# Performance work log

Hardware: AMD Instinct MI355X
Metric: run time of the kernel (lower is better)

## Reference

```python
import jax, jax.numpy as jnp
import numpy as np

B, CIN, CF, FH, FW = 16, 512, 64, 11, 20
N = 2784          # anchors
NOFF = 72         # S offsets
D = CF * FH       # 704

def setup_inputs() -> dict:
    key = jax.random.key(0)
    ks = jax.random.split(key, 12)
    x = jax.random.normal(ks[0], (B, CIN, FH, FW), jnp.float32)
    conv_w = jax.random.normal(ks[1], (CF, CIN), jnp.float32) * 0.02
    conv_b = jax.random.normal(ks[2], (CF,), jnp.float32) * 0.01
    attn_w = jax.random.normal(ks[3], (N - 1, D), jnp.float32) * 0.02
    attn_b = jnp.zeros((N - 1,), jnp.float32)
    cls_w = jax.random.normal(ks[4], (2, 2 * D), jnp.float32) * 0.02
    cls_b = jnp.zeros((2,), jnp.float32)
    reg_w = jax.random.normal(ks[5], (NOFF + 1, 2 * D), jnp.float32) * 0.02
    reg_b = jnp.zeros((NOFF + 1,), jnp.float32)
    anchors = jax.random.normal(ks[6], (N, 5 + NOFF), jnp.float32)
    # emulate compute_anchor_cut_indices: per-anchor per-fmap-row x index, some invalid
    unclamped = jax.random.randint(ks[7], (N, FH), -3, FW + 3, jnp.int32)
    invalid_mask = (unclamped < 0) | (unclamped > FW)
    cut_xs = jnp.clip(unclamped, 0, FW - 1).astype(jnp.int32)
    return {"x": x, "conv_w": conv_w, "conv_b": conv_b, "attn_w": attn_w,
            "attn_b": attn_b, "cls_w": cls_w, "cls_b": cls_b, "reg_w": reg_w,
            "reg_b": reg_b, "anchors": anchors, "cut_xs": cut_xs,
            "invalid_mask": invalid_mask}

def reference(x, conv_w, conv_b, attn_w, attn_b, cls_w, cls_b, reg_w, reg_b,
              anchors, cut_xs, invalid_mask):
    # 1x1 conv: [B, CF, FH, FW]
    feat = jnp.einsum('bchw,oc->bohw', x, conv_w) + conv_b[None, :, None, None]
    # cut_anchor_features: gather per-anchor column of features, mask invalid
    ys = jnp.arange(FH)[None, :]                      # [1, FH] broadcasts with cut_xs [N, FH]
    rois = feat[:, :, ys, cut_xs]                     # [B, CF, N, FH]
    rois = jnp.where(invalid_mask[None, None], 0.0, rois)
    anchor_feat = jnp.transpose(rois, (0, 2, 1, 3)).reshape(B, N, D)  # (C-major, then H)
    # attention scores over other anchors
    scores = anchor_feat.reshape(B * N, D) @ attn_w.T + attn_b
    att = jax.nn.softmax(scores, axis=1).reshape(B, N, N - 1)
    # build NxN matrix: zero diagonal, off-diagonal filled row-wise with att
    r = jnp.arange(N)[:, None]
    c = jnp.arange(N)[None, :]
    k = jnp.clip(c - (c > r).astype(jnp.int32), 0, N - 2)  # [N, N]
    M = att[:, r, k] * (c != r)                       # [B, N, N]
    att_feat = jnp.einsum('bij,bjd->bid', M, anchor_feat)
    comb = jnp.concatenate([att_feat, anchor_feat], axis=-1)  # [B, N, 2D]
    cls = comb @ cls_w.T + cls_b                      # [B, N, 2]
    reg = comb @ reg_w.T + reg_b                      # [B, N, 73]
    mid = jnp.broadcast_to(anchors[None, :, 2:4], (B, N, 2))
    props = jnp.concatenate([cls, mid, anchors[None, :, 4:] + reg], axis=-1)  # [B, N, 77]
    return props, M
```

## Files before the change

kernel.cpp:

```cpp
#include <hip/hip_runtime.h>

#define B_    16
#define CIN_  512
#define CF_   64
#define FH_   11
#define FW_   20
#define N_    2784
#define NM1_  2783
#define D_    704
#define D2_   1408
#define ROWS_ 44544
#define PW_   77

#define NX_     1802240
#define NCW_    32768
#define NCB_    64
#define NATTW_  1959232
#define NATTB_  2783
#define NCLSW_  2816
#define NCLSB_  2
#define NREGW_  102784
#define NREGB_  73
#define NANCH_  214368
#define NCUT_   30624

#define OFF_FLAGS   0u
#define OFF_FEAT    256u
#define OFF_CANON   (1u<<20)
#define C_X      0u
#define C_ATTW   3604480u
#define C_CW     7522944u
#define C_ANCH   7588480u
#define C_CLSW   8017216u
#define C_REGW   8022848u
#define C_CB     8228416u
#define C_ATTB   8228544u
#define C_CLSB   8234112u
#define C_REGB   8234128u
#define C_CUT    8234288u
#define C_MASK   8356784u

typedef __bf16 bf16x8 __attribute__((ext_vector_type(8)));
typedef float  f32x4  __attribute__((ext_vector_type(4)));

typedef __attribute__((address_space(1))) void g_void;
typedef __attribute__((address_space(3))) void l_void;
#define GLD16(gp, lp) __builtin_amdgcn_global_load_lds((g_void*)(gp), (l_void*)(lp), 16, 0, 0)

__device__ __forceinline__ float bf2f(unsigned short u) {
    union { unsigned int u; float f; } v; v.u = ((unsigned int)u) << 16; return v.f;
}
__device__ __forceinline__ unsigned short f2bf(float f) {
    union { float f; unsigned int u; } v; v.f = f;
    unsigned int x = v.u;
    return (unsigned short)((x + 0x7FFFu + ((x >> 16) & 1u)) >> 16);
}

__device__ __forceinline__ int swz8(int olid, int nwg) {
    int xcd = olid & 7, pos = olid >> 3;
    int q = nwg >> 3, r = nwg & 7;
    int off = (xcd < r) ? xcd * (q + 1) : r * (q + 1) + (xcd - r) * q;
    return off + pos;
}

__global__ __launch_bounds__(256) void k_detect(const unsigned int* __restrict__ attw,
                                                const unsigned int* __restrict__ cut,
                                                const unsigned int* __restrict__ msk,
                                                int* __restrict__ flags) {
    __shared__ int cnt[3];
    int t = threadIdx.x;
    if (t < 3) cnt[t] = 0;
    __syncthreads();
    int c0 = 0, c1 = 0, c2 = 0;
    for (int i = t; i < 2048; i += 256) {
        unsigned int e = (attw[i] >> 7) & 0xFFu;
        if (e >= 127u) c0++;
    }
    for (int i = t; i < 4096; i += 256) if (cut[i] >= 32u) c1++;
    for (int i = t; i < 4096; i += 256) if (msk[i] >= 2u)  c2++;
    atomicAdd(&cnt[0], c0); atomicAdd(&cnt[1], c1); atomicAdd(&cnt[2], c2);
    __syncthreads();
    if (t == 0) {
        flags[0] = cnt[0] > 64;
        flags[1] = cnt[1] > 64;
        flags[2] = cnt[2] > 64;
        flags[3] = 0;
    }
}

__device__ __forceinline__ void cvt_arr(const void* s, unsigned short* d, int n, int isf32,
                                        int tid, int stride) {
    if (isf32) {
        const float* p = (const float*)s;
        for (int i = tid; i < n; i += stride) d[i] = f2bf(p[i]);
    } else {
        const unsigned short* p = (const unsigned short*)s;
        for (int i = tid; i < n; i += stride) d[i] = p[i];
    }
}

__global__ __launch_bounds__(256) void k_canon_f(const void* sx, const void* scw, const void* scb,
                                                 const void* sattw, const void* sattb,
                                                 const void* sclsw, const void* sclsb,
                                                 const void* sregw, const void* sregb,
                                                 const void* sanch, char* canon,
                                                 const int* __restrict__ flags) {
    const int isf32 = flags[0];
    const int tid = blockIdx.x * 256 + threadIdx.x;
    const int stride = gridDim.x * 256;
    cvt_arr(sx,    (unsigned short*)(canon + C_X),    NX_,    isf32, tid, stride);
    cvt_arr(sattw, (unsigned short*)(canon + C_ATTW), NATTW_, isf32, tid, stride);
    cvt_arr(scw,   (unsigned short*)(canon + C_CW),   NCW_,   isf32, tid, stride);
    cvt_arr(sanch, (unsigned short*)(canon + C_ANCH), NANCH_, isf32, tid, stride);
    cvt_arr(sclsw, (unsigned short*)(canon + C_CLSW), NCLSW_, isf32, tid, stride);
    cvt_arr(sregw, (unsigned short*)(canon + C_REGW), NREGW_, isf32, tid, stride);
    cvt_arr(scb,   (unsigned short*)(canon + C_CB),   NCB_,   isf32, tid, stride);
    cvt_arr(sattb, (unsigned short*)(canon + C_ATTB), NATTB_, isf32, tid, stride);
    cvt_arr(sclsb, (unsigned short*)(canon + C_CLSB), NCLSB_, isf32, tid, stride);
    cvt_arr(sregb, (unsigned short*)(canon + C_REGB), NREGB_, isf32, tid, stride);
}

__global__ __launch_bounds__(256) void k_canon_i(const void* scut, const void* smsk,
                                                 char* canon, const int* __restrict__ flags) {
    const int cutb = flags[1], mskb = flags[2];
    int* ccut = (int*)(canon + C_CUT);
    int* cmsk = (int*)(canon + C_MASK);
    const int tid = blockIdx.x * 256 + threadIdx.x;
    const int stride = gridDim.x * 256;
    for (int i = tid; i < NCUT_; i += stride) {
        ccut[i] = cutb ? (int)((const unsigned char*)scut)[i] : ((const int*)scut)[i];
        int m = mskb ? (int)((const unsigned char*)smsk)[i] : ((const int*)smsk)[i];
        cmsk[i] = (m != 0);
    }
}

__global__ __launch_bounds__(256) void k_conv(const unsigned short* __restrict__ x,
                                              const unsigned short* __restrict__ cw,
                                              const unsigned short* __restrict__ cb,
                                              float* __restrict__ feat) {
    int idx = blockIdx.x * 256 + threadIdx.x;
    int w = idx % FW_;
    int h = (idx / FW_) % FH_;
    int o = (idx / (FW_ * FH_)) % CF_;
    int b = idx / (FW_ * FH_ * CF_);
    const unsigned short* xp = x + ((size_t)(b * CIN_) * FH_ + h) * FW_ + w;
    const unsigned short* wp = cw + (size_t)o * CIN_;
    float acc = bf2f(cb[o]);
#pragma unroll 8
    for (int c = 0; c < CIN_; ++c)
        acc += bf2f(xp[(size_t)c * (FH_ * FW_)]) * bf2f(wp[c]);
    feat[idx] = acc;
}

__global__ __launch_bounds__(256) void k_gather_af(const float* __restrict__ feat,
                                                   const int* __restrict__ cut,
                                                   const int* __restrict__ inv,
                                                   unsigned short* __restrict__ AF,
                                                   int batch_base) {
    int n = blockIdx.x, bl = blockIdx.y;
    int b = batch_base + bl;
    __shared__ int cu[FH_];
    __shared__ int iv[FH_];
    int t = threadIdx.x;
    if (t < FH_) { cu[t] = cut[n * FH_ + t]; iv[t] = inv[n * FH_ + t]; }
    __syncthreads();
    unsigned short* out = AF + ((size_t)(bl * N_ + n)) * D_;
    for (int d = t; d < D_; d += 256) {
        int c = d / FH_, h = d - c * FH_;
        float v = iv[h] ? 0.f : feat[((b * CF_ + c) * FH_ + h) * FW_ + cu[h]];
        out[d] = f2bf(v);
    }
}

__global__ __launch_bounds__(256) void k_gather_aft(const float* __restrict__ feat,
                                                    const int* __restrict__ cut,
                                                    const int* __restrict__ inv,
                                                    unsigned short* __restrict__ AFT,
                                                    int batch_base) {
    int d = blockIdx.x, bl = blockIdx.y;
    int b = batch_base + bl;
    int c = d / FH_, h = d - c * FH_;
    const float* fp = feat + ((b * CF_ + c) * FH_ + h) * FW_;
    unsigned short* out = AFT + ((size_t)(bl * D_ + d)) * N_;
    for (int n = threadIdx.x; n < N_; n += 256) {
        int w = cut[n * FH_ + h];
        float v = inv[n * FH_ + h] ? 0.f : fp[w];
        out[n] = f2bf(v);
    }
}

__global__ __launch_bounds__(256, 2) void k_scores(const unsigned short* __restrict__ AF,
                                                   const unsigned short* __restrict__ attw,
                                                   const unsigned short* __restrict__ attb,
                                                   unsigned short* __restrict__ Mbf,
                                                   int nloc) {
    __shared__ __bf16 As[2][256 * 32];
    __shared__ __bf16 Bs[2][128 * 32];
    const int t = threadIdx.x;
    const int nwg = gridDim.x * gridDim.y;
    const int olid = blockIdx.x + gridDim.x * blockIdx.y;
    const int nid = swz8(olid, nwg);
    const int jt = nid % 22, it = nid / 22;
    const int i0 = it * 256, j0 = jt * 128;
    const int lane = t & 63, wv = t >> 6;
    const int wrow = wv >> 1, wcol = wv & 1;
    const int l15 = lane & 15;
    const int hix = (((lane >> 4) ^ ((l15 >> 1) & 3)) * 8);

    f32x4 zero = {0.f, 0.f, 0.f, 0.f};
    f32x4 acc[8][4];
#pragma unroll
    for (int m = 0; m < 8; ++m)
#pragma unroll
        for (int n = 0; n < 4; ++n) acc[m][n] = zero;

    const unsigned short* aP[4];
    const unsigned short* bP[2];
#pragma unroll
    for (int k = 0; k < 4; ++k) {
        int s = t + 256 * k;
        int row = s >> 2;
        int ac = (((s & 3) ^ ((s >> 3) & 3)) * 8);
        int ir = i0 + row; if (ir > nloc - 1) ir = nloc - 1;
        aP[k] = AF + (size_t)ir * D_ + ac;
    }
#pragma unroll
    for (int k = 0; k < 2; ++k) {
        int s = t + 256 * k;
        int row = s >> 2;
        int ac = (((s & 3) ^ ((s >> 3) & 3)) * 8);
        int jr = j0 + row; if (jr > NM1_ - 1) jr = NM1_ - 1;
        bP[k] = attw + (size_t)jr * D_ + ac;
    }

    const int NT = D_ / 32;
#pragma unroll
    for (int k = 0; k < 4; ++k) GLD16(aP[k], As[0] + (t + 256 * k) * 8);
#pragma unroll
    for (int k = 0; k < 2; ++k) GLD16(bP[k], Bs[0] + (t + 256 * k) * 8);

    for (int kt = 0; kt < NT; ++kt) {
        const int cur = kt & 1;
        if (kt + 1 < NT) {
            const int nk = (kt + 1) * 32;
#pragma unroll
            for (int k = 0; k < 4; ++k) GLD16(aP[k] + nk, As[cur ^ 1] + (t + 256 * k) * 8);
#pragma unroll
            for (int k = 0; k < 2; ++k) GLD16(bP[k] + nk, Bs[cur ^ 1] + (t + 256 * k) * 8);
            asm volatile("s_waitcnt vmcnt(6)" ::: "memory");
        } else {
            asm volatile("s_waitcnt vmcnt(0)" ::: "memory");
        }
        __builtin_amdgcn_sched_barrier(0);
        __builtin_amdgcn_s_barrier();
        bf16x8 a[8], bb[4];
#pragma unroll
        for (int m = 0; m < 8; ++m)
            a[m] = *(const bf16x8*)(As[cur] + (wrow * 128 + m * 16 + l15) * 32 + hix);
#pragma unroll
        for (int n = 0; n < 4; ++n)
            bb[n] = *(const bf16x8*)(Bs[cur] + (wcol * 64 + n * 16 + l15) * 32 + hix);
#pragma unroll
        for (int m = 0; m < 8; ++m)
#pragma unroll
            for (int n = 0; n < 4; ++n)
                acc[m][n] = __builtin_amdgcn_mfma_f32_16x16x32_bf16(a[m], bb[n], acc[m][n], 0, 0, 0);
        __builtin_amdgcn_s_barrier();
        __builtin_amdgcn_sched_barrier(0);
    }

#pragma unroll
    for (int m = 0; m < 8; ++m) {
        int ib = i0 + wrow * 128 + m * 16 + (lane >> 4) * 4;
#pragma unroll
        for (int n = 0; n < 4; ++n) {
            int j = j0 + wcol * 64 + n * 16 + l15;
            if (j < NM1_) {
                float bias = bf2f(attb[j]);
#pragma unroll
                for (int q = 0; q < 4; ++q) {
                    int ii = ib + q;
                    if (ii < nloc) {
                        int r = ii % N_;
                        int c = j + (j >= r);
                        Mbf[(size_t)ii * N_ + c] = f2bf(acc[m][n][q] + bias);
                    }
                }
            }
        }
    }
}

__global__ __launch_bounds__(256) void k_softmax(unsigned short* __restrict__ Mbf,
                                                 float* __restrict__ Mout,
                                                 int row_base) {
    const int il = blockIdx.x;
    const int r = il % N_;
    unsigned short* srow = Mbf + (size_t)il * N_;
    float* orow = Mout + (size_t)(row_base + il) * N_;
    const int t = threadIdx.x;
    float f[16];
#pragma unroll
    for (int q = 0; q < 2; ++q) {
        int c8 = t + 256 * q;
        if (c8 < N_ / 8) {
            uint4 u = *(const uint4*)(srow + c8 * 8);
            const unsigned short* pu = (const unsigned short*)&u;
#pragma unroll
            for (int e = 0; e < 8; ++e) {
                int c = c8 * 8 + e;
                float v = bf2f(pu[e]);
                f[q * 8 + e] = (c == r) ? -1e30f : v;
            }
        } else {
#pragma unroll
            for (int e = 0; e < 8; ++e) f[q * 8 + e] = -1e30f;
        }
    }
    float m = -1e30f;
#pragma unroll
    for (int q = 0; q < 16; ++q) m = fmaxf(m, f[q]);
#pragma unroll
    for (int off = 32; off >= 1; off >>= 1) m = fmaxf(m, __shfl_xor(m, off, 64));
    __shared__ float red[4];
    if ((t & 63) == 0) red[t >> 6] = m;
    __syncthreads();
    m = fmaxf(fmaxf(red[0], red[1]), fmaxf(red[2], red[3]));

    float s = 0.f;
#pragma unroll
    for (int q = 0; q < 16; ++q) { float e = __expf(f[q] - m); f[q] = e; s += e; }
#pragma unroll
    for (int off = 32; off >= 1; off >>= 1) s += __shfl_xor(s, off, 64);
    __shared__ float red2[4];
    if ((t & 63) == 0) red2[t >> 6] = s;
    __syncthreads();
    s = red2[0] + red2[1] + red2[2] + red2[3];
    float inv = 1.0f / s;
#pragma unroll
    for (int q = 0; q < 2; ++q) {
        int c8 = t + 256 * q;
        if (c8 < N_ / 8) {
            float o[8];
            union { unsigned short u[8]; uint4 v; } pb;
#pragma unroll
            for (int e = 0; e < 8; ++e) {
                o[e] = f[q * 8 + e] * inv;
                pb.u[e] = f2bf(o[e]);
            }
            float4 o0 = {o[0], o[1], o[2], o[3]};
            float4 o1 = {o[4], o[5], o[6], o[7]};
            *(float4*)(orow + c8 * 8) = o0;
            *(float4*)(orow + c8 * 8 + 4) = o1;
            *(uint4*)(srow + c8 * 8) = pb.v;
        }
    }
}

__global__ __launch_bounds__(256, 2) void k_attgemm(const unsigned short* __restrict__ Mbf,
                                                    const unsigned short* __restrict__ AFT,
                                                    unsigned short* __restrict__ ATF) {
    __shared__ __bf16 As[2][256 * 32];
    __shared__ __bf16 Bs[2][128 * 32];
    const int t = threadIdx.x;
    const int nwg = gridDim.x * gridDim.y * gridDim.z;
    const int olid = blockIdx.x + gridDim.x * (blockIdx.y + gridDim.y * blockIdx.z);
    const int nid = swz8(olid, nwg);
    const int jt = nid % 6, it = (nid / 6) % 11, bl = nid / 66;
    const int i0 = it * 256, j0 = jt * 128;
    const int lane = t & 63, wv = t >> 6;
    const int wrow = wv >> 1, wcol = wv & 1;
    const int l15 = lane & 15;
    const int hix = (((lane >> 4) ^ ((l15 >> 1) & 3)) * 8);

    f32x4 zero = {0.f, 0.f, 0.f, 0.f};
    f32x4 acc[8][4];
#pragma unroll
    for (int m = 0; m < 8; ++m)
#pragma unroll
        for (int n = 0; n < 4; ++n) acc[m][n] = zero;

    const unsigned short* aP[4];
    const unsigned short* bP[2];
#pragma unroll
    for (int k = 0; k < 4; ++k) {
        int s = t + 256 * k;
        int row = s >> 2;
        int ac = (((s & 3) ^ ((s >> 3) & 3)) * 8);
        int ir = i0 + row; if (ir > N_ - 1) ir = N_ - 1;
        aP[k] = Mbf + ((size_t)bl * N_ + ir) * N_ + ac;
    }
#pragma unroll
    for (int k = 0; k < 2; ++k) {
        int s = t + 256 * k;
        int row = s >> 2;
        int ac = (((s & 3) ^ ((s >> 3) & 3)) * 8);
        int jr = j0 + row; if (jr > D_ - 1) jr = D_ - 1;
        bP[k] = AFT + (size_t)(bl * D_ + jr) * N_ + ac;
    }

    const int NT = N_ / 32;
#pragma unroll
    for (int k = 0; k < 4; ++k) GLD16(aP[k], As[0] + (t + 256 * k) * 8);
#pragma unroll
    for (int k = 0; k < 2; ++k) GLD16(bP[k], Bs[0] + (t + 256 * k) * 8);

    for (int kt = 0; kt < NT; ++kt) {
        const int cur = kt & 1;
        if (kt + 1 < NT) {
            const int nk = (kt + 1) * 32;
#pragma unroll
            for (int k = 0; k < 4; ++k) GLD16(aP[k] + nk, As[cur ^ 1] + (t + 256 * k) * 8);
#pragma unroll
            for (int k = 0; k < 2; ++k) GLD16(bP[k] + nk, Bs[cur ^ 1] + (t + 256 * k) * 8);
            asm volatile("s_waitcnt vmcnt(6)" ::: "memory");
        } else {
            asm volatile("s_waitcnt vmcnt(0)" ::: "memory");
        }
        __builtin_amdgcn_sched_barrier(0);
        __builtin_amdgcn_s_barrier();
        bf16x8 a[8], bb[4];
#pragma unroll
        for (int m = 0; m < 8; ++m)
            a[m] = *(const bf16x8*)(As[cur] + (wrow * 128 + m * 16 + l15) * 32 + hix);
#pragma unroll
        for (int n = 0; n < 4; ++n)
            bb[n] = *(const bf16x8*)(Bs[cur] + (wcol * 64 + n * 16 + l15) * 32 + hix);
#pragma unroll
        for (int m = 0; m < 8; ++m)
#pragma unroll
            for (int n = 0; n < 4; ++n)
                acc[m][n] = __builtin_amdgcn_mfma_f32_16x16x32_bf16(a[m], bb[n], acc[m][n], 0, 0, 0);
        __builtin_amdgcn_s_barrier();
        __builtin_amdgcn_sched_barrier(0);
    }

#pragma unroll
    for (int m = 0; m < 8; ++m) {
        int rb = i0 + wrow * 128 + m * 16 + (lane >> 4) * 4;
#pragma unroll
        for (int n = 0; n < 4; ++n) {
            int d = j0 + wcol * 64 + n * 16 + l15;
            if (d < D_) {
#pragma unroll
                for (int q = 0; q < 4; ++q) {
                    int rr = rb + q;
                    if (rr < N_)
                        ATF[((size_t)(bl * N_ + rr)) * D_ + d] = f2bf(acc[m][n][q]);
                }
            }
        }
    }
}

__global__ __launch_bounds__(256) void k_head(const unsigned short* __restrict__ ATF,
                                              const unsigned short* __restrict__ AF,
                                              const unsigned short* __restrict__ clsw,
                                              const unsigned short* __restrict__ clsb,
                                              const unsigned short* __restrict__ regw,
                                              const unsigned short* __restrict__ regb,
                                              const unsigned short* __restrict__ anch,
                                              float* __restrict__ props,
                                              int row_base, int nloc) {
    __shared__ __bf16 As[128 * 32];
    __shared__ __bf16 Ws[80 * 32];
    const int t = threadIdx.x;
    const int i0 = blockIdx.x * 128;
    const int lane = t & 63, wv = t >> 6;
    const int l15 = lane & 15, hi8 = (lane >> 4) * 8;

    f32x4 zero = {0.f, 0.f, 0.f, 0.f};
    f32x4 acc[2][5];
#pragma unroll
    for (int m = 0; m < 2; ++m)
#pragma unroll
        for (int n = 0; n < 5; ++n) acc[m][n] = zero;

    const int s0 = t, s1 = t + 256;
    const int ar0 = s0 >> 2, ac0 = (s0 & 3) * 8;
    const int ar1 = s1 >> 2, ac1 = (s1 & 3) * 8;
    int ir0 = i0 + ar0; if (ir0 > nloc - 1) ir0 = nloc - 1;
    int ir1 = i0 + ar1; if (ir1 > nloc - 1) ir1 = nloc - 1;
    const unsigned short* w0base = (ar0 < 2) ? (clsw + (size_t)ar0 * D2_)
                                             : (regw + (size_t)(ar0 - 2) * D2_);
    int r1 = 64 + (t >> 2);
    int rc = r1 < 75 ? r1 : 74;
    const unsigned short* w1base = regw + (size_t)(rc - 2) * D2_;
    const int w1c = (t & 3) * 8;

    for (int p = 0; p < 2; ++p) {
        const unsigned short* Asrc = (p == 0) ? ATF : AF;
        const int wcol = p * D_;
        for (int k0 = 0; k0 < D_; k0 += 32) {
            GLD16(Asrc + (size_t)ir0 * D_ + ac0 + k0, As + s0 * 8);
            GLD16(Asrc + (size_t)ir1 * D_ + ac1 + k0, As + s1 * 8);
            GLD16(w0base + wcol + k0 + ac0, Ws + s0 * 8);
            if (t < 64) GLD16(w1base + wcol + k0 + w1c, Ws + (size_t)(256 + t) * 8);
            __syncthreads();
            bf16x8 a[2], bb[5];
#pragma unroll
            for (int m = 0; m < 2; ++m)
                a[m] = *(const bf16x8*)(As + (wv * 32 + m * 16 + l15) * 32 + hi8);
#pragma unroll
            for (int n = 0; n < 5; ++n)
                bb[n] = *(const bf16x8*)(Ws + (n * 16 + l15) * 32 + hi8);
#pragma unroll
            for (int m = 0; m < 2; ++m)
#pragma unroll
                for (int n = 0; n < 5; ++n)
                    acc[m][n] = __builtin_amdgcn_mfma_f32_16x16x32_bf16(a[m], bb[n], acc[m][n], 0, 0, 0);
            __syncthreads();
        }
    }

#pragma unroll
    for (int m = 0; m < 2; ++m) {
        int ib = i0 + wv * 32 + m * 16 + (lane >> 4) * 4;
#pragma unroll
        for (int n = 0; n < 5; ++n) {
            int j = n * 16 + l15;
            if (j < 75) {
#pragma unroll
                for (int q = 0; q < 4; ++q) {
                    int i = ib + q;
                    if (i < nloc) {
                        size_t g = (size_t)(row_base + i);
                        int nn = i % N_;
                        float v = acc[m][n][q];
                        if (j < 2) {
                            props[g * PW_ + j] = v + bf2f(clsb[j]);
                            props[g * PW_ + 2 + j] = bf2f(anch[(size_t)nn * PW_ + 2 + j]);
                        } else {
                            int tt = j - 2;
                            props[g * PW_ + 4 + tt] = v + bf2f(regb[tt]) + bf2f(anch[(size_t)nn * PW_ + 4 + tt]);
                        }
                    }
                }
            }
        }
    }
}

extern "C" void kernel_launch(void* const* d_in, const int* in_sizes, int n_in,
                              void* d_out, int out_size, void* d_ws, size_t ws_size,
                              hipStream_t stream) {
    (void)in_sizes; (void)n_in; (void)out_size;

    float* props = (float*)d_out;
    float* Mbuf  = props + (size_t)ROWS_ * PW_;

    char* ws = (char*)d_ws;
    int* flags = (int*)(ws + OFF_FLAGS);
    float* feat = (float*)(ws + OFF_FEAT);
    char* canon = ws + OFF_CANON;
    unsigned short* cx    = (unsigned short*)(canon + C_X);
    unsigned short* cattw = (unsigned short*)(canon + C_ATTW);
    unsigned short* ccw   = (unsigned short*)(canon + C_CW);
    unsigned short* canch = (unsigned short*)(canon + C_ANCH);
    unsigned short* cclsw = (unsigned short*)(canon + C_CLSW);
    unsigned short* cregw = (unsigned short*)(canon + C_REGW);
    unsigned short* ccb   = (unsigned short*)(canon + C_CB);
    unsigned short* cattb = (unsigned short*)(canon + C_ATTB);
    unsigned short* cclsb = (unsigned short*)(canon + C_CLSB);
    unsigned short* cregb = (unsigned short*)(canon + C_REGB);
    int* ccut = (int*)(canon + C_CUT);
    int* cmsk = (int*)(canon + C_MASK);

    const size_t base = (size_t)(12u << 20);
    const size_t sAF  = (size_t)N_ * D_ * 2;
    const size_t sMB  = (size_t)N_ * N_ * 2;
    const size_t per  = 3 * sAF + sMB;
    int CN = 1;
    for (int c = 16; c >= 1; c >>= 1)
        if (ws_size >= base + (size_t)c * per) { CN = c; break; }
    unsigned short* AF  = (unsigned short*)(ws + base);
    unsigned short* AFT = AF  + (size_t)CN * N_ * D_;
    unsigned short* ATF = AFT + (size_t)CN * N_ * D_;
    unsigned short* Mbf = ATF + (size_t)CN * N_ * D_;

    k_detect<<<dim3(1), dim3(256), 0, stream>>>((const unsigned int*)d_in[3],
                                                (const unsigned int*)d_in[10],
                                                (const unsigned int*)d_in[11], flags);
    k_canon_f<<<dim3(1024), dim3(256), 0, stream>>>(d_in[0], d_in[1], d_in[2], d_in[3], d_in[4],
                                                    d_in[5], d_in[6], d_in[7], d_in[8], d_in[9],
                                                    canon, flags);
    k_canon_i<<<dim3(120), dim3(256), 0, stream>>>(d_in[10], d_in[11], canon, flags);
    k_conv<<<dim3(880), dim3(256), 0, stream>>>(cx, ccw, ccb, feat);

    const int nchunk = 16 / CN;
    for (int c = 0; c < nchunk; ++c) {
        const int bb = c * CN;
        const int rb = bb * N_;
        const int nl = CN * N_;
        const int it128 = (nl + 127) / 128;
        const int it256 = (nl + 255) / 256;
        const int atiles = (N_ + 255) / 256;
        k_gather_af<<<dim3(N_, CN), dim3(256), 0, stream>>>(feat, ccut, cmsk, AF, bb);
        k_gather_aft<<<dim3(D_, CN), dim3(256), 0, stream>>>(feat, ccut, cmsk, AFT, bb);
        k_scores<<<dim3(22, it256), dim3(256), 0, stream>>>(AF, cattw, cattb, Mbf, nl);
        k_softmax<<<dim3(nl), dim3(256), 0, stream>>>(Mbf, Mbuf, rb);
        k_attgemm<<<dim3(6, atiles, CN), dim3(256), 0, stream>>>(Mbf, AFT, ATF);
        k_head<<<dim3(it128), dim3(256), 0, stream>>>(ATF, AF, cclsw, cclsb, cregw, cregb,
                                                      canch, props, rb, nl);
    }
}
```

Before: 1.067 ms.

## Enlarge GEMM tiles to 256x256x64 with 512 threads and pad K to 2816

Both MFMA GEMMs (scores and attention-feature) move from 256x128 tiles with a K step of 32 and 256 threads to 256x256 tiles with a K step of 64, 512 threads and 8 waves. The LDS layout gets a new XOR swizzle for the wider rows. The Mbf and AFT buffers are padded to a row stride of 2816, with zero-filled tails written by softmax and gather, so the attention GEMM K loop divides evenly into 64-wide steps. The intent is more data reuse per loaded tile and fewer barriers per FLOP. In exchange it uses 128KB of LDS per block, runs one block per CU, and waits on vmcnt(0) at every step, which may reduce latency hiding.

New measurement: 1.097 ms. 1.03x slower.

```diff
diff --git a/kernel.cpp b/kernel.cpp
--- a/kernel.cpp
+++ b/kernel.cpp
@@ -7,6 +7,7 @@
 #define FW_   20
 #define N_    2784
 #define NM1_  2783
+#define PK_   2816
 #define D_    704
 #define D2_   1408
 #define ROWS_ 44544
@@ -181,31 +182,33 @@
     int b = batch_base + bl;
     int c = d / FH_, h = d - c * FH_;
     const float* fp = feat + ((b * CF_ + c) * FH_ + h) * FW_;
-    unsigned short* out = AFT + ((size_t)(bl * D_ + d)) * N_;
-    for (int n = threadIdx.x; n < N_; n += 256) {
-        int w = cut[n * FH_ + h];
-        float v = inv[n * FH_ + h] ? 0.f : fp[w];
+    unsigned short* out = AFT + ((size_t)(bl * D_ + d)) * PK_;
+    for (int n = threadIdx.x; n < PK_; n += 256) {
+        float v = 0.f;
+        if (n < N_) {
+            int w = cut[n * FH_ + h];
+            v = inv[n * FH_ + h] ? 0.f : fp[w];
+        }
         out[n] = f2bf(v);
     }
 }
 
-__global__ __launch_bounds__(256, 2) void k_scores(const unsigned short* __restrict__ AF,
+__global__ __launch_bounds__(512, 1) void k_scores(const unsigned short* __restrict__ AF,
                                                    const unsigned short* __restrict__ attw,
                                                    const unsigned short* __restrict__ attb,
                                                    unsigned short* __restrict__ Mbf,
                                                    int nloc) {
-    __shared__ __bf16 As[2][256 * 32];
-    __shared__ __bf16 Bs[2][128 * 32];
+    __shared__ __bf16 As[2][256 * 64];
+    __shared__ __bf16 Bs[2][256 * 64];
     const int t = threadIdx.x;
     const int nwg = gridDim.x * gridDim.y;
     const int olid = blockIdx.x + gridDim.x * blockIdx.y;
     const int nid = swz8(olid, nwg);
-    const int jt = nid % 22, it = nid / 22;
-    const int i0 = it * 256, j0 = jt * 128;
+    const int jt = nid % 11, it = nid / 11;
+    const int i0 = it * 256, j0 = jt * 256;
     const int lane = t & 63, wv = t >> 6;
-    const int wrow = wv >> 1, wcol = wv & 1;
-    const int l15 = lane & 15;
-    const int hix = (((lane >> 4) ^ ((l15 >> 1) & 3)) * 8);
+    const int wrow = wv >> 2, wcol = wv & 3;
+    const int l15 = lane & 15, hi = lane >> 4;
 
     f32x4 zero = {0.f, 0.f, 0.f, 0.f};
     f32x4 acc[8][4];
@@ -215,63 +218,68 @@
         for (int n = 0; n < 4; ++n) acc[m][n] = zero;
 
     const unsigned short* aP[4];
-    const unsigned short* bP[2];
+    const unsigned short* bP[4];
 #pragma unroll
     for (int k = 0; k < 4; ++k) {
-        int s = t + 256 * k;
-        int row = s >> 2;
-        int ac = (((s & 3) ^ ((s >> 3) & 3)) * 8);
+        int s = t + 512 * k;
+        int row = s >> 3;
+        int lc = (s & 7) ^ (row & 7);
         int ir = i0 + row; if (ir > nloc - 1) ir = nloc - 1;
-        aP[k] = AF + (size_t)ir * D_ + ac;
-    }
-#pragma unroll
-    for (int k = 0; k < 2; ++k) {
-        int s = t + 256 * k;
-        int row = s >> 2;
-        int ac = (((s & 3) ^ ((s >> 3) & 3)) * 8);
+        aP[k] = AF + (size_t)ir * D_ + lc * 8;
         int jr = j0 + row; if (jr > NM1_ - 1) jr = NM1_ - 1;
-        bP[k] = attw + (size_t)jr * D_ + ac;
-    }
-
-    const int NT = D_ / 32;
-#pragma unroll
-    for (int k = 0; k < 4; ++k) GLD16(aP[k], As[0] + (t + 256 * k) * 8);
-#pragma unroll
-    for (int k = 0; k < 2; ++k) GLD16(bP[k], Bs[0] + (t + 256 * k) * 8);
-
+        bP[k] = attw + (size_t)jr * D_ + lc * 8;
+    }
+
+    const int NT = D_ / 64;
+#pragma unroll
+    for (int k = 0; k < 4; ++k) {
+        GLD16(aP[k], As[0] + (t + 512 * k) * 8);
+        GLD16(bP[k], Bs[0] + (t + 512 * k) * 8);
+    }
+    asm volatile("s_waitcnt vmcnt(0)" ::: "memory");
+    __builtin_amdgcn_sched_barrier(0);
+    __builtin_amdgcn_s_barrier();
+
+    int cur = 0;
     for (int kt = 0; kt < NT; ++kt) {
-        const int cur = kt & 1;
         if (kt + 1 < NT) {
-            const int nk = (kt + 1) * 32;
-#pragma unroll
-            for (int k = 0; k < 4; ++k) GLD16(aP[k] + nk, As[cur ^ 1] + (t + 256 * k) * 8);
-#pragma unroll
-            for (int k = 0; k < 2; ++k) GLD16(bP[k] + nk, Bs[cur ^ 1] + (t + 256 * k) * 8);
-            asm volatile("s_waitcnt vmcnt(6)" ::: "memory");
-        } else {
-            asm volatile("s_waitcnt vmcnt(0)" ::: "memory");
-        }
+            const int nk = (kt + 1) * 64;
+#pragma unroll
+            for (int k = 0; k < 4; ++k) {
+                GLD16(aP[k] + nk, As[cur ^ 1] + (t + 512 * k) * 8);
+                GLD16(bP[k] + nk, Bs[cur ^ 1] + (t + 512 * k) * 8);
+            }
+        }
+#pragma unroll
+        for (int h = 0; h < 2; ++h) {
+            bf16x8 a[8], bb[4];
+#pragma unroll
+            for (int m = 0; m < 8; ++m) {
+                int R = wrow * 128 + m * 16 + l15;
+                int pc = (hi + 4 * h) ^ (R & 7);
+                a[m] = *(const bf16x8*)(As[cur] + R * 64 + pc * 8);
+            }
+#pragma unroll
+            for (int n = 0; n < 4; ++n) {
+                int R = wcol * 64 + n * 16 + l15;
+                int pc = (hi + 4 * h) ^ (R & 7);
+                bb[n] = *(const bf16x8*)(Bs[cur] + R * 64 + pc * 8);
+            }
+#pragma unroll
+            for (int m = 0; m < 8; ++m)
+#pragma unroll
+                for (int n = 0; n < 4; ++n)
+                    acc[m][n] = __builtin_amdgcn_mfma_f32_16x16x32_bf16(a[m], bb[n], acc[m][n], 0, 0, 0);
+        }
+        asm volatile("s_waitcnt vmcnt(0)" ::: "memory");
         __builtin_amdgcn_sched_barrier(0);
         __builtin_amdgcn_s_barrier();
-        bf16x8 a[8], bb[4];
-#pragma unroll
-        for (int m = 0; m < 8; ++m)
-            a[m] = *(const bf16x8*)(As[cur] + (wrow * 128 + m * 16 + l15) * 32 + hix);
-#pragma unroll
-        for (int n = 0; n < 4; ++n)
-            bb[n] = *(const bf16x8*)(Bs[cur] + (wcol * 64 + n * 16 + l15) * 32 + hix);
-#pragma unroll
-        for (int m = 0; m < 8; ++m)
-#pragma unroll
-            for (int n = 0; n < 4; ++n)
-                acc[m][n] = __builtin_amdgcn_mfma_f32_16x16x32_bf16(a[m], bb[n], acc[m][n], 0, 0, 0);
-        __builtin_amdgcn_s_barrier();
-        __builtin_amdgcn_sched_barrier(0);
+        cur ^= 1;
     }
 
 #pragma unroll
     for (int m = 0; m < 8; ++m) {
-        int ib = i0 + wrow * 128 + m * 16 + (lane >> 4) * 4;
+        int ib = i0 + wrow * 128 + m * 16 + hi * 4;
 #pragma unroll
         for (int n = 0; n < 4; ++n) {
             int j = j0 + wcol * 64 + n * 16 + l15;
@@ -283,7 +291,7 @@
                     if (ii < nloc) {
                         int r = ii % N_;
                         int c = j + (j >= r);
-                        Mbf[(size_t)ii * N_ + c] = f2bf(acc[m][n][q] + bias);
+                        Mbf[(size_t)ii * PK_ + c] = f2bf(acc[m][n][q] + bias);
                     }
                 }
             }
@@ -296,7 +304,7 @@
                                                  int row_base) {
     const int il = blockIdx.x;
     const int r = il % N_;
-    unsigned short* srow = Mbf + (size_t)il * N_;
+    unsigned short* srow = Mbf + (size_t)il * PK_;
     float* orow = Mout + (size_t)(row_base + il) * N_;
     const int t = threadIdx.x;
     float f[16];
@@ -355,23 +363,26 @@
             *(uint4*)(srow + c8 * 8) = pb.v;
         }
     }
-}
-
-__global__ __launch_bounds__(256, 2) void k_attgemm(const unsigned short* __restrict__ Mbf,
+    if (t < 4) {
+        uint4 z = {0u, 0u, 0u, 0u};
+        *(uint4*)(srow + N_ + t * 8) = z;
+    }
+}
+
+__global__ __launch_bounds__(512, 1) void k_attgemm(const unsigned short* __restrict__ Mbf,
                                                     const unsigned short* __restrict__ AFT,
                                                     unsigned short* __restrict__ ATF) {
-    __shared__ __bf16 As[2][256 * 32];
-    __shared__ __bf16 Bs[2][128 * 32];
+    __shared__ __bf16 As[2][256 * 64];
+    __shared__ __bf16 Bs[2][256 * 64];
     const int t = threadIdx.x;
     const int nwg = gridDim.x * gridDim.y * gridDim.z;
     const int olid = blockIdx.x + gridDim.x * (blockIdx.y + gridDim.y * blockIdx.z);
     const int nid = swz8(olid, nwg);
-    const int jt = nid % 6, it = (nid / 6) % 11, bl = nid / 66;
-    const int i0 = it * 256, j0 = jt * 128;
+    const int jt = nid % 3, it = (nid / 3) % 11, bl = nid / 33;
+    const int i0 = it * 256, j0 = jt * 256;
     const int lane = t & 63, wv = t >> 6;
-    const int wrow = wv >> 1, wcol = wv & 1;
-    const int l15 = lane & 15;
-    const int hix = (((lane >> 4) ^ ((l15 >> 1) & 3)) * 8);
+    const int wrow = wv >> 2, wcol = wv & 3;
+    const int l15 = lane & 15, hi = lane >> 4;
 
     f32x4 zero = {0.f, 0.f, 0.f, 0.f};
     f32x4 acc[8][4];
@@ -381,63 +392,68 @@
         for (int n = 0; n < 4; ++n) acc[m][n] = zero;
 
     const unsigned short* aP[4];
-    const unsigned short* bP[2];
+    const unsigned short* bP[4];
 #pragma unroll
     for (int k = 0; k < 4; ++k) {
-        int s = t + 256 * k;
-        int row = s >> 2;
-        int ac = (((s & 3) ^ ((s >> 3) & 3)) * 8);
+        int s = t + 512 * k;
+        int row = s >> 3;
+        int lc = (s & 7) ^ (row & 7);
         int ir = i0 + row; if (ir > N_ - 1) ir = N_ - 1;
-        aP[k] = Mbf + ((size_t)bl * N_ + ir) * N_ + ac;
-    }
-#pragma unroll
-    for (int k = 0; k < 2; ++k) {
-        int s = t + 256 * k;
-        int row = s >> 2;
-        int ac = (((s & 3) ^ ((s >> 3) & 3)) * 8);
+        aP[k] = Mbf + ((size_t)bl * N_ + ir) * PK_ + lc * 8;
         int jr = j0 + row; if (jr > D_ - 1) jr = D_ - 1;
-        bP[k] = AFT + (size_t)(bl * D_ + jr) * N_ + ac;
-    }
-
-    const int NT = N_ / 32;
-#pragma unroll
-    for (int k = 0; k < 4; ++k) GLD16(aP[k], As[0] + (t + 256 * k) * 8);
-#pragma unroll
-    for (int k = 0; k < 2; ++k) GLD16(bP[k], Bs[0] + (t + 256 * k) * 8);
-
+        bP[k] = AFT + ((size_t)bl * D_ + jr) * PK_ + lc * 8;
+    }
+
+    const int NT = PK_ / 64;
+#pragma unroll
+    for (int k = 0; k < 4; ++k) {
+        GLD16(aP[k], As[0] + (t + 512 * k) * 8);
+        GLD16(bP[k], Bs[0] + (t + 512 * k) * 8);
+    }
+    asm volatile("s_waitcnt vmcnt(0)" ::: "memory");
+    __builtin_amdgcn_sched_barrier(0);
+    __builtin_amdgcn_s_barrier();
+
+    int cur = 0;
     for (int kt = 0; kt < NT; ++kt) {
-        const int cur = kt & 1;
         if (kt + 1 < NT) {
-            const int nk = (kt + 1) * 32;
-#pragma unroll
-            for (int k = 0; k < 4; ++k) GLD16(aP[k] + nk, As[cur ^ 1] + (t + 256 * k) * 8);
-#pragma unroll
-            for (int k = 0; k < 2; ++k) GLD16(bP[k] + nk, Bs[cur ^ 1] + (t + 256 * k) * 8);
-            asm volatile("s_waitcnt vmcnt(6)" ::: "memory");
-        } else {
-            asm volatile("s_waitcnt vmcnt(0)" ::: "memory");
-        }
+            const int nk = (kt + 1) * 64;
+#pragma unroll
+            for (int k = 0; k < 4; ++k) {
+                GLD16(aP[k] + nk, As[cur ^ 1] + (t + 512 * k) * 8);
+                GLD16(bP[k] + nk, Bs[cur ^ 1] + (t + 512 * k) * 8);
+            }
+        }
+#pragma unroll
+        for (int h = 0; h < 2; ++h) {
+            bf16x8 a[8], bb[4];
+#pragma unroll
+            for (int m = 0; m < 8; ++m) {
+                int R = wrow * 128 + m * 16 + l15;
+                int pc = (hi + 4 * h) ^ (R & 7);
+                a[m] = *(const bf16x8*)(As[cur] + R * 64 + pc * 8);
+            }
+#pragma unroll
+            for (int n = 0; n < 4; ++n) {
+                int R = wcol * 64 + n * 16 + l15;
+                int pc = (hi + 4 * h) ^ (R & 7);
+                bb[n] = *(const bf16x8*)(Bs[cur] + R * 64 + pc * 8);
+            }
+#pragma unroll
+            for (int m = 0; m < 8; ++m)
+#pragma unroll
+                for (int n = 0; n < 4; ++n)
+                    acc[m][n] = __builtin_amdgcn_mfma_f32_16x16x32_bf16(a[m], bb[n], acc[m][n], 0, 0, 0);
+        }
+        asm volatile("s_waitcnt vmcnt(0)" ::: "memory");
         __builtin_amdgcn_sched_barrier(0);
         __builtin_amdgcn_s_barrier();
-        bf16x8 a[8], bb[4];
-#pragma unroll
-        for (int m = 0; m < 8; ++m)
-            a[m] = *(const bf16x8*)(As[cur] + (wrow * 128 + m * 16 + l15) * 32 + hix);
-#pragma unroll
-        for (int n = 0; n < 4; ++n)
-            bb[n] = *(const bf16x8*)(Bs[cur] + (wcol * 64 + n * 16 + l15) * 32 + hix);
-#pragma unroll
-        for (int m = 0; m < 8; ++m)
-#pragma unroll
-            for (int n = 0; n < 4; ++n)
-                acc[m][n] = __builtin_amdgcn_mfma_f32_16x16x32_bf16(a[m], bb[n], acc[m][n], 0, 0, 0);
-        __builtin_amdgcn_s_barrier();
-        __builtin_amdgcn_sched_barrier(0);
+        cur ^= 1;
     }
 
 #pragma unroll
     for (int m = 0; m < 8; ++m) {
-        int rb = i0 + wrow * 128 + m * 16 + (lane >> 4) * 4;
+        int rb = i0 + wrow * 128 + m * 16 + hi * 4;
 #pragma unroll
         for (int n = 0; n < 4; ++n) {
             int d = j0 + wcol * 64 + n * 16 + l15;
@@ -567,15 +583,13 @@
     int* cmsk = (int*)(canon + C_MASK);
 
     const size_t base = (size_t)(12u << 20);
-    const size_t sAF  = (size_t)N_ * D_ * 2;
-    const size_t sMB  = (size_t)N_ * N_ * 2;
-    const size_t per  = 3 * sAF + sMB;
+    const size_t per  = ((size_t)N_ * D_ * 2) * 2 + (size_t)D_ * PK_ * 2 + (size_t)N_ * PK_ * 2;
     int CN = 1;
     for (int c = 16; c >= 1; c >>= 1)
         if (ws_size >= base + (size_t)c * per) { CN = c; break; }
     unsigned short* AF  = (unsigned short*)(ws + base);
     unsigned short* AFT = AF  + (size_t)CN * N_ * D_;
-    unsigned short* ATF = AFT + (size_t)CN * N_ * D_;
+    unsigned short* ATF = AFT + (size_t)CN * D_ * PK_;
     unsigned short* Mbf = ATF + (size_t)CN * N_ * D_;
 
     k_detect<<<dim3(1), dim3(256), 0, stream>>>((const unsigned int*)d_in[3],
@@ -594,12 +608,11 @@
         const int nl = CN * N_;
         const int it128 = (nl + 127) / 128;
         const int it256 = (nl + 255) / 256;
-        const int atiles = (N_ + 255) / 256;
         k_gather_af<<<dim3(N_, CN), dim3(256), 0, stream>>>(feat, ccut, cmsk, AF, bb);
         k_gather_aft<<<dim3(D_, CN), dim3(256), 0, stream>>>(feat, ccut, cmsk, AFT, bb);
-        k_scores<<<dim3(22, it256), dim3(256), 0, stream>>>(AF, cattw, cattb, Mbf, nl);
+        k_scores<<<dim3(11, it256), dim3(512), 0, stream>>>(AF, cattw, cattb, Mbf, nl);
         k_softmax<<<dim3(nl), dim3(256), 0, stream>>>(Mbf, Mbuf, rb);
-        k_attgemm<<<dim3(6, atiles, CN), dim3(256), 0, stream>>>(Mbf, AFT, ATF);
+        k_attgemm<<<dim3(3, 11, CN), dim3(512), 0, stream>>>(Mbf, AFT, ATF);
         k_head<<<dim3(it128), dim3(256), 0, stream>>>(ATF, AF, cclsw, cclsb, cregw, cregb,
                                                       canch, props, rb, nl);
     }
```
